# Kernel optimization log

Hardware: AMD Instinct MI355X
Metric: run time of the kernel (lower is better)

The kernel has to match this reference:

```python
import jax, jax.numpy as jnp
import numpy as np

B, S, D, H = 2, 2048, 1024, 16
HD = D // H  # head_dim = 64
NEG_INF = -jnp.inf


def _rope_tables(seq_len, head_dim, theta=10000.0):
    inv = 1.0 / (theta ** (np.arange(0, head_dim, 2, dtype=np.float32) / head_dim))
    t = np.arange(seq_len, dtype=np.float32)
    ang = np.outer(t, inv)  # [S, HD/2]
    return jnp.asarray(np.cos(ang)), jnp.asarray(np.sin(ang))


def _apply_rope(x, cos, sin):
    # x: [B, S, H, HD]; pairs (even, odd) rotated by complex freqs, matching
    # torch.view_as_complex(reshape(..., -1, 2)) * freqs_cis.
    x2 = x.reshape(*x.shape[:-1], HD // 2, 2)
    x0, x1 = x2[..., 0], x2[..., 1]
    c = cos[None, :, None, :]
    s = sin[None, :, None, :]
    o0 = x0 * c - x1 * s
    o1 = x0 * s + x1 * c
    return jnp.stack([o0, o1], axis=-1).reshape(x.shape)


def setup_inputs() -> dict:
    key = jax.random.key(0)
    ks = jax.random.split(key, 10)
    sc = 1.0 / np.sqrt(D)
    return {
        "x": jax.random.normal(ks[0], (B, S, D), dtype=jnp.float32),
        "effective_len": jax.random.randint(ks[1], (B,), 0, 1024, dtype=jnp.int32),
        "Wq": jax.random.normal(ks[2], (D, D), dtype=jnp.float32) * sc,
        "bq": jnp.zeros((D,), dtype=jnp.float32),
        "Wk": jax.random.normal(ks[3], (D, D), dtype=jnp.float32) * sc,
        "bk": jnp.zeros((D,), dtype=jnp.float32),
        "Wv": jax.random.normal(ks[4], (D, D), dtype=jnp.float32) * sc,
        "bv": jnp.zeros((D,), dtype=jnp.float32),
        "Wo": jax.random.normal(ks[5], (D, D), dtype=jnp.float32) * sc,
        "bo": jnp.zeros((D,), dtype=jnp.float32),
    }


def reference(x, effective_len, Wq, bq, Wk, bk, Wv, bv, Wo, bo):
    cos, sin = _rope_tables(S, HD)
    q = (x @ Wq.T + bq).reshape(B, S, H, HD)
    k = (x @ Wk.T + bk).reshape(B, S, H, HD)
    v = (x @ Wv.T + bv).reshape(B, S, H, HD)
    q = _apply_rope(q, cos, sin)
    k = _apply_rope(k, cos, sin)
    # [B, H, S, S]
    scores = jnp.einsum("bqhd,bkhd->bhqk", q, k) / np.sqrt(HD)
    row = jnp.arange(S)[:, None]
    col = jnp.arange(S)[None, :]
    causal = jnp.where(col > row, NEG_INF, 0.0)  # [S, S]
    scores = scores + causal[None, None, :, :]
    # faithful replication of original: masks the LAST effective_len key columns
    pad = jnp.where(col[None, 0, :] >= (S - effective_len)[:, None], NEG_INF, 0.0)  # [B, S]
    scores = scores + pad[:, None, None, :]
    probs = jax.nn.softmax(scores.astype(jnp.float32), axis=-1).astype(x.dtype)
    out = jnp.einsum("bhqk,bkhd->bqhd", probs, v).reshape(B, S, D)
    return out @ Wo.T + bo  # dropout in eval mode = identity
```

## Files before the change

### kernel.cpp

```cpp
#include <hip/hip_runtime.h>

#define SB   2048
#define DD   1024
#define NH   16
#define HDIM 64
#define NB   2

typedef float f4 __attribute__((ext_vector_type(4)));
typedef __bf16 bf16x8 __attribute__((ext_vector_type(8)));
typedef unsigned short u16;
typedef unsigned int u32;
typedef unsigned long long u64;
typedef u16 u16x8 __attribute__((ext_vector_type(8)));
typedef u16 u16x4 __attribute__((ext_vector_type(4)));

#define QSCALE 0.1803368801111f

__device__ __forceinline__ u16 f2bf(float f) {
  unsigned u = __float_as_uint(f);
  u += 0x7FFFu + ((u >> 16) & 1u);
  return (u16)(u >> 16);
}

typedef __attribute__((address_space(3))) unsigned int lds_uint;
typedef __attribute__((address_space(1))) const unsigned int glb_uint;
__device__ __forceinline__ void gl_lds16(const void* g, void* l) {
  __builtin_amdgcn_global_load_lds((glb_uint*)g, (lds_uint*)l, 16, 0, 0);
}

__device__ __forceinline__ void cvt8(const float* __restrict__ src,
                                     u16* __restrict__ dst, size_t i) {
  f4 a = *(const f4*)(src + 8 * i);
  f4 b = *(const f4*)(src + 8 * i + 4);
  u16x8 o;
  o[0] = f2bf(a[0]); o[1] = f2bf(a[1]); o[2] = f2bf(a[2]); o[3] = f2bf(a[3]);
  o[4] = f2bf(b[0]); o[5] = f2bf(b[1]); o[6] = f2bf(b[2]); o[7] = f2bf(b[3]);
  *(u16x8*)(dst + 8 * i) = o;
}

__global__ __launch_bounds__(256) void prep_kernel(
    const float* __restrict__ x, const float* __restrict__ Wq,
    const float* __restrict__ Wk, const float* __restrict__ Wv,
    const float* __restrict__ Wo,
    u16* __restrict__ xb, u16* __restrict__ Wb3, u16* __restrict__ WoB,
    float* __restrict__ cosT, float* __restrict__ sinT, int nwo) {
  int bid = blockIdx.x, t = threadIdx.x;
  if (bid < 2048) {
    cvt8(x, xb, (size_t)bid * 256 + t);
  } else if (bid < 2560) {
    cvt8(Wq, Wb3, (size_t)(bid - 2048) * 256 + t);
  } else if (bid < 3072) {
    cvt8(Wk, Wb3 + (1u << 20), (size_t)(bid - 2560) * 256 + t);
  } else if (bid < 3584) {
    cvt8(Wv, Wb3 + (2u << 20), (size_t)(bid - 3072) * 256 + t);
  } else if (bid < 3584 + nwo) {
    cvt8(Wo, WoB, (size_t)(bid - 3584) * 256 + t);
  } else {
    int idx = (bid - 3584 - nwo) * 256 + t;
    int tt = idx & 31, s = idx >> 5;
    float inv = powf(10000.0f, -2.0f * (float)tt / 64.0f);
    float ang = (float)s * inv;
    cosT[idx] = cosf(ang);
    sinT[idx] = sinf(ang);
  }
}

__global__ __launch_bounds__(256) void cvt_bf16_kernel(const float* __restrict__ src,
                                                       u16* __restrict__ dst) {
  cvt8(src, dst, (size_t)blockIdx.x * 256 + threadIdx.x);
}

__global__ __launch_bounds__(256, 4) void gemm_qkv_fused_kernel(
    const u16* __restrict__ A, const u16* __restrict__ W3,
    const float* __restrict__ bq, const float* __restrict__ bk,
    const float* __restrict__ bv,
    u16* __restrict__ Qw, u16* __restrict__ Kw, u16* __restrict__ Vt,
    const float* __restrict__ cosT, const float* __restrict__ sinT) {
  const int K = DD;
  __shared__ char smem[32768];
  u16* As = (u16*)smem;
  u16* Bs = (u16*)(smem + 16384);
  const int t = threadIdx.x;
  const int wave = t >> 6, lane = t & 63;
  const int m0 = blockIdx.x * 128, n0 = blockIdx.y * 128;
  const int mw = (wave >> 1) * 64, nw = (wave & 1) * 64;
  const int quad = lane >> 4, l15 = lane & 15;
  const int srow = lane >> 3, sgran = lane & 7;
  const u16* Ab = A + (size_t)m0 * K;
  const u16* Bb = W3 + (size_t)n0 * K;
  f4 acc[4][4];
#pragma unroll
  for (int i = 0; i < 4; i++)
#pragma unroll
    for (int j = 0; j < 4; j++) acc[i][j] = (f4)0.f;

  for (int kt = 0; kt < K; kt += 64) {
#pragma unroll
    for (int is = 0; is < 4; is++) {
      int r = wave * 32 + is * 8 + srow;
      int lg = sgran ^ (r & 7);
      gl_lds16(Ab + (size_t)r * K + kt + lg * 8, &As[(wave * 32 + is * 8) * 64]);
      gl_lds16(Bb + (size_t)r * K + kt + lg * 8, &Bs[(wave * 32 + is * 8) * 64]);
    }
    __syncthreads();
#pragma unroll
    for (int kh = 0; kh < 2; kh++) {
      bf16x8 af[4], bfr[4];
#pragma unroll
      for (int i = 0; i < 4; i++) {
        int R = mw + 16 * i + l15;
        af[i] = *(const bf16x8*)&As[R * 64 + ((kh * 4 + quad) ^ (R & 7)) * 8];
        int Rb = nw + 16 * i + l15;
        bfr[i] = *(const bf16x8*)&Bs[Rb * 64 + ((kh * 4 + quad) ^ (Rb & 7)) * 8];
      }
#pragma unroll
      for (int i = 0; i < 4; i++)
#pragma unroll
        for (int j = 0; j < 4; j++)
          acc[i][j] = __builtin_amdgcn_mfma_f32_16x16x32_bf16(af[i], bfr[j],
                                                              acc[i][j], 0, 0, 0);
    }
    __syncthreads();
  }

  const int which = n0 >> 10;
  const int hh = ((n0 & 1023) + nw) >> 6;
  const int cb = (n0 + nw) & 1023;

  if (which == 2) {
#pragma unroll
    for (int j = 0; j < 4; j++) {
      const int dh = 16 * j + l15;
      const float bval = bv[cb + 16 * j + l15];
#pragma unroll
      for (int a = 0; a < 2; a++) {
        int mg0 = m0 + mw + 32 * a;
        int b = mg0 >> 11, sr0 = mg0 & (SB - 1);
        u16x8 o;
#pragma unroll
        for (int r = 0; r < 4; r++) o[r] = f2bf(acc[2 * a][j][r] + bval);
#pragma unroll
        for (int r = 0; r < 4; r++) o[4 + r] = f2bf(acc[2 * a + 1][j][r] + bval);
        *(u16x8*)(Vt + ((size_t)(b * NH + hh) * HDIM + dh) * SB +
                  (sr0 | (quad << 3))) = o;
      }
    }
  } else {
    u16* dst = which ? Kw : Qw;
    const float* barr = which ? bk : bq;
    const float scale = which ? 1.0f : QSCALE;
    float bvj[4];
#pragma unroll
    for (int j = 0; j < 4; j++) bvj[j] = barr[cb + 16 * j + l15];
    float* sl = (float*)(smem + wave * 8192);
    const int kk = lane >> 1, hf = lane & 1;
#pragma unroll
    for (int half = 0; half < 2; half++) {
#pragma unroll
      for (int il = 0; il < 2; il++) {
#pragma unroll
        for (int j = 0; j < 4; j++) {
          const int q = 4 * j + (l15 >> 2);
          const int w = l15 & 3;
#pragma unroll
          for (int r = 0; r < 4; r++) {
            const int row = il * 16 + quad * 4 + r;
            sl[(row << 6) + (((q + row) & 15) << 2) + w] =
                (acc[half * 2 + il][j][r] + bvj[j]) * scale;
          }
        }
      }
      asm volatile("s_waitcnt lgkmcnt(0)" ::: "memory");
      const int m = m0 + mw + half * 32 + kk;
      const int b = m >> 11, sr = m & (SB - 1);
      const float* ct = cosT + sr * 32 + hf * 16;
      const float* st2 = sinT + sr * 32 + hf * 16;
      u16* op = dst + (((size_t)(b * NH + hh)) * SB + sr) * HDIM + hf * 32;
#pragma unroll
      for (int q8 = 0; q8 < 4; q8++) {
        f4 c4 = *(const f4*)(ct + q8 * 4);
        f4 s4 = *(const f4*)(st2 + q8 * 4);
        const int qc0 = hf * 8 + q8 * 2;
        f4 v0 = *(const f4*)(sl + (kk << 6) + (((qc0 + kk) & 15) << 2));
        f4 v1 = *(const f4*)(sl + (kk << 6) + (((qc0 + 1 + kk) & 15) << 2));
        u16x8 o;
        o[0] = f2bf(v0[0] * c4[0] - v0[1] * s4[0]);
        o[1] = f2bf(v0[0] * s4[0] + v0[1] * c4[0]);
        o[2] = f2bf(v0[2] * c4[1] - v0[3] * s4[1]);
        o[3] = f2bf(v0[2] * s4[1] + v0[3] * c4[1]);
        o[4] = f2bf(v1[0] * c4[2] - v1[1] * s4[2]);
        o[5] = f2bf(v1[0] * s4[2] + v1[1] * c4[2]);
        o[6] = f2bf(v1[2] * c4[3] - v1[3] * s4[3]);
        o[7] = f2bf(v1[2] * s4[3] + v1[3] * c4[3]);
        *(u16x8*)(op + q8 * 8) = o;
      }
      if (half == 0) asm volatile("s_waitcnt lgkmcnt(0)" ::: "memory");
    }
  }
}

__global__ __launch_bounds__(256) void gemm_out_kernel(
    const u16* __restrict__ A, const u16* __restrict__ W,
    const float* __restrict__ bias, float* __restrict__ outp) {
  const int K = DD;
  __shared__ u16 As[128 * 64];
  __shared__ u16 Bs[64 * 64];
  const int t = threadIdx.x;
  const int wave = t >> 6, lane = t & 63;
  const int m0 = blockIdx.x * 128, n0 = blockIdx.y * 64;
  const int mw = (wave >> 1) * 64, nw = (wave & 1) * 32;
  const int quad = lane >> 4, l15 = lane & 15;
  const int srow = lane >> 3, sgran = lane & 7;
  const u16* Ab = A + (size_t)m0 * K;
  const u16* Bb = W + (size_t)n0 * K;
  f4 acc[4][2];
#pragma unroll
  for (int i = 0; i < 4; i++)
#pragma unroll
    for (int j = 0; j < 2; j++) acc[i][j] = (f4)0.f;

  for (int kt = 0; kt < K; kt += 64) {
#pragma unroll
    for (int is = 0; is < 4; is++) {
      int r = wave * 32 + is * 8 + srow;
      int lg = sgran ^ (r & 7);
      gl_lds16(Ab + (size_t)r * K + kt + lg * 8, &As[(wave * 32 + is * 8) * 64]);
    }
#pragma unroll
    for (int is = 0; is < 2; is++) {
      int r = wave * 16 + is * 8 + srow;
      int lg = sgran ^ (r & 7);
      gl_lds16(Bb + (size_t)r * K + kt + lg * 8, &Bs[(wave * 16 + is * 8) * 64]);
    }
    __syncthreads();
#pragma unroll
    for (int kh = 0; kh < 2; kh++) {
      bf16x8 af[4], bfr[2];
#pragma unroll
      for (int i = 0; i < 4; i++) {
        int R = mw + 16 * i + l15;
        af[i] = *(const bf16x8*)&As[R * 64 + ((kh * 4 + quad) ^ (R & 7)) * 8];
      }
#pragma unroll
      for (int j = 0; j < 2; j++) {
        int R = nw + 16 * j + l15;
        bfr[j] = *(const bf16x8*)&Bs[R * 64 + ((kh * 4 + quad) ^ (R & 7)) * 8];
      }
#pragma unroll
      for (int i = 0; i < 4; i++)
#pragma unroll
        for (int j = 0; j < 2; j++)
          acc[i][j] = __builtin_amdgcn_mfma_f32_16x16x32_bf16(af[i], bfr[j],
                                                              acc[i][j], 0, 0, 0);
    }
    __syncthreads();
  }
#pragma unroll
  for (int i = 0; i < 4; i++)
#pragma unroll
    for (int j = 0; j < 2; j++) {
      int colg = n0 + nw + 16 * j + l15;
#pragma unroll
      for (int r = 0; r < 4; r++) {
        int mg = m0 + mw + 16 * i + quad * 4 + r;
        outp[(size_t)mg * DD + colg] = acc[i][j][r] + bias[colg];
      }
    }
}

__global__ __launch_bounds__(512) void attn_mfma_kernel(
    const u16* __restrict__ Qw, const u16* __restrict__ Kw,
    const u16* __restrict__ Vt, u16* __restrict__ Ow,
    const int* __restrict__ eff) {
  __shared__ u16 KL[2][8 * 64 * 8];
  __shared__ u16 VL[2][8 * 64 * 8];
  const int w = threadIdx.x >> 6, lane = threadIdx.x & 63;
  const int l15 = lane & 15, q4 = lane >> 4;
  const int lid = blockIdx.x;
  const int qp = lid >> 5;
  const int c  = lid & 31;
  const int h = c & 15, b = c >> 4;
  const int wg = w >> 2, wl = w & 3;
  const int QT = wg ? (SB / 128 - 1 - qp) : qp;
  const int limit = SB - eff[b];
  const size_t bh = ((size_t)b * NH + h) * (SB * HDIM);

  const int rowbase = QT * 128 + wl * 32;

  bf16x8 qf[2][2];
  {
    const u16* qp0 = Qw + bh + (size_t)(rowbase + l15) * HDIM + q4 * 8;
    qf[0][0] = *(const bf16x8*)qp0;
    qf[0][1] = *(const bf16x8*)(qp0 + 32);
    const u16* qp1 = qp0 + 16 * HDIM;
    qf[1][0] = *(const bf16x8*)qp1;
    qf[1][1] = *(const bf16x8*)(qp1 + 32);
  }

  f4 acc[2][4];
#pragma unroll
  for (int s = 0; s < 2; s++)
#pragma unroll
    for (int dt = 0; dt < 4; dt++) acc[s][dt] = (f4)0.f;
  float l_run[2] = {0.f, 0.f};

  const int kendB = min((SB / 128 - 1 - qp) * 128 + 127, limit - 1);
  const int ntiles = (kendB >> 6) + 1;
  const int wkend = min(rowbase + 31, limit - 1);

#define STAGE_TILE(TILE, BUF)                                                   \
  {                                                                             \
    const int colb_ = (TILE) * 64;                                              \
    _Pragma("unroll") for (int f = 0; f < 2; f++) {                             \
      int fr = w * 2 + f;                                                       \
      if (fr < 8) {                                                             \
        int mt = fr >> 1, j = fr & 1;                                           \
        gl_lds16(Kw + bh + (size_t)(colb_ + mt * 16 + l15) * HDIM + q4 * 8 + j * 32, \
                 &KL[BUF][fr * 512]);                                           \
      } else {                                                                  \
        int fv = fr - 8, dt = fv >> 1, j = fv & 1;                              \
        gl_lds16(Vt + bh + (size_t)(dt * 16 + l15) * SB + colb_ + q4 * 8 + j * 32, \
                 &VL[BUF][fv * 512]);                                           \
      }                                                                         \
    }                                                                           \
  }

  STAGE_TILE(0, 0)
  __syncthreads();

  for (int kt = 0; kt < ntiles; kt++) {
    const int cur = kt & 1;
    const int colb = kt * 64;
    if (kt + 1 < ntiles) STAGE_TILE(kt + 1, cur ^ 1)

    if (colb <= wkend) {
      f4 sa[2][4];
      __builtin_amdgcn_s_setprio(1);
#pragma unroll
      for (int mt = 0; mt < 4; mt++) {
        bf16x8 k0 = *(const bf16x8*)&KL[cur][(mt * 2 + 0) * 512 + lane * 8];
        bf16x8 k1 = *(const bf16x8*)&KL[cur][(mt * 2 + 1) * 512 + lane * 8];
        f4 s0 = (f4)0.f, s1 = (f4)0.f;
        s0 = __builtin_amdgcn_mfma_f32_16x16x32_bf16(k0, qf[0][0], s0, 0, 0, 0);
        s0 = __builtin_amdgcn_mfma_f32_16x16x32_bf16(k1, qf[0][1], s0, 0, 0, 0);
        s1 = __builtin_amdgcn_mfma_f32_16x16x32_bf16(k0, qf[1][0], s1, 0, 0, 0);
        s1 = __builtin_amdgcn_mfma_f32_16x16x32_bf16(k1, qf[1][1], s1, 0, 0, 0);
        sa[0][mt] = s0;
        sa[1][mt] = s1;
      }
      __builtin_amdgcn_s_setprio(0);

      u32 pk[2][4][2];
#pragma unroll
      for (int s = 0; s < 2; s++) {
        const int rb = rowbase + 16 * s;
        const int rg = rb + l15;
        const bool needmask = (colb + 63 > rb) || (colb + 63 >= limit);
        if (needmask) {
#pragma unroll
          for (int mt = 0; mt < 4; mt++)
#pragma unroll
            for (int r = 0; r < 4; r++) {
              int col = colb + mt * 16 + q4 * 4 + r;
              if (col > rg || col >= limit) sa[s][mt][r] = -3.0e38f;
            }
        }
        float lsum = 0.f;
#pragma unroll
        for (int mt = 0; mt < 4; mt++) {
          float p0 = exp2f(sa[s][mt][0]);
          float p1 = exp2f(sa[s][mt][1]);
          float p2 = exp2f(sa[s][mt][2]);
          float p3 = exp2f(sa[s][mt][3]);
          lsum += (p0 + p1) + (p2 + p3);
          pk[s][mt][0] = (__float_as_uint(p1) & 0xFFFF0000u) | (__float_as_uint(p0) >> 16);
          pk[s][mt][1] = (__float_as_uint(p3) & 0xFFFF0000u) | (__float_as_uint(p2) >> 16);
        }
        l_run[s] += lsum;
      }

      union { u32 wds[4]; bf16x8 v; } ub[2][2];
#pragma unroll
      for (int s = 0; s < 2; s++) {
        ub[s][0].wds[0] = pk[s][0][0]; ub[s][0].wds[1] = pk[s][0][1];
        ub[s][0].wds[2] = pk[s][1][0]; ub[s][0].wds[3] = pk[s][1][1];
        ub[s][1].wds[0] = pk[s][2][0]; ub[s][1].wds[1] = pk[s][2][1];
        ub[s][1].wds[2] = pk[s][3][0]; ub[s][1].wds[3] = pk[s][3][1];
      }
      __builtin_amdgcn_s_setprio(1);
#pragma unroll
      for (int dt = 0; dt < 4; dt++) {
        bf16x8 v0 = *(const bf16x8*)&VL[cur][(dt * 2 + 0) * 512 + lane * 8];
        bf16x8 v1 = *(const bf16x8*)&VL[cur][(dt * 2 + 1) * 512 + lane * 8];
#pragma unroll
        for (int s = 0; s < 2; s++) {
          acc[s][dt] = __builtin_amdgcn_mfma_f32_16x16x32_bf16(v0, ub[s][0].v, acc[s][dt], 0, 0, 0);
          acc[s][dt] = __builtin_amdgcn_mfma_f32_16x16x32_bf16(v1, ub[s][1].v, acc[s][dt], 0, 0, 0);
        }
      }
      __builtin_amdgcn_s_setprio(0);
    }
    __syncthreads();
  }

#pragma unroll
  for (int s = 0; s < 2; s++) {
    float lt = l_run[s];
    lt += __shfl_xor(lt, 16);
    lt += __shfl_xor(lt, 32);
    const float linv = 1.0f / lt;
    const int rg = rowbase + 16 * s + l15;
    const size_t obase = (((size_t)b * SB + rg) * NH + h) * HDIM + q4 * 4;
#pragma unroll
    for (int dt = 0; dt < 4; dt++) {
      u16x4 o;
      o[0] = f2bf(acc[s][dt][0] * linv);
      o[1] = f2bf(acc[s][dt][1] * linv);
      o[2] = f2bf(acc[s][dt][2] * linv);
      o[3] = f2bf(acc[s][dt][3] * linv);
      *(u16x4*)(Ow + obase + dt * 16) = o;
    }
  }
}

extern "C" void kernel_launch(void* const* d_in, const int* in_sizes, int n_in,
                              void* d_out, int out_size, void* d_ws, size_t ws_size,
                              hipStream_t stream) {
  (void)in_sizes; (void)n_in; (void)out_size;
  const float* x  = (const float*)d_in[0];
  const int*   eff = (const int*)d_in[1];
  const float* Wq = (const float*)d_in[2];
  const float* bq = (const float*)d_in[3];
  const float* Wk = (const float*)d_in[4];
  const float* bk = (const float*)d_in[5];
  const float* Wv = (const float*)d_in[6];
  const float* bv = (const float*)d_in[7];
  const float* Wo = (const float*)d_in[8];
  const float* bo = (const float*)d_in[9];
  float* out = (float*)d_out;

  char* ws = (char*)d_ws;
  u16* Qw = (u16*)(ws);
  u16* Kw = (u16*)(ws + (8u << 20));
  u16* Vt = (u16*)(ws + (16u << 20));
  u16* Ow = (u16*)(ws + (24u << 20));
  u16* xb = (u16*)(ws + (24u << 20));
  u16* Wb3 = (u16*)(ws + (32u << 20));
  float* cosT = (float*)(ws + (38u << 20));
  float* sinT = (float*)(ws + (38u << 20) + (256u << 10));

  size_t wob_off = (38u << 20) + (512u << 10);
  int nwo = (ws_size >= wob_off + (2u << 20)) ? 512 : 0;
  u16* WoB = nwo ? (u16*)(ws + wob_off) : Wb3;

  hipLaunchKernelGGL(prep_kernel, dim3(3840 + nwo), dim3(256), 0, stream,
                     x, Wq, Wk, Wv, Wo, xb, Wb3, WoB, cosT, sinT, nwo);

  hipLaunchKernelGGL(gemm_qkv_fused_kernel, dim3(32, 24), dim3(256), 0, stream,
                     xb, Wb3, bq, bk, bv, Qw, Kw, Vt, cosT, sinT);

  if (!nwo)
    hipLaunchKernelGGL(cvt_bf16_kernel, dim3(512), dim3(256), 0, stream, Wo, WoB);

  hipLaunchKernelGGL(attn_mfma_kernel, dim3(256), dim3(512), 0, stream,
                     Qw, Kw, Vt, Ow, eff);

  hipLaunchKernelGGL(gemm_out_kernel, dim3(32, 16), dim3(256), 0, stream, Ow, WoB, bo, out);
}
```

Baseline: 191.2 us.

## Double-buffer QKV GEMM LDS tiles with K-step 32 to overlap loads and MFMA

The fused QKV projection GEMM now uses two LDS buffers of 128x32 A/B tiles and prefetches the next K-slice while computing on the current one, instead of loading a 64-wide K tile and synchronizing before compute. The LDS swizzle changes to a 4-granule XOR pattern to match the narrower tiles. The goal is to hide global-to-LDS latency behind the MFMA work. In exchange there are twice as many loop iterations and barriers, and each iteration does less compute, which may not cover the load latency.

Result: slower. 198.9 us (+4.0%).

```diff
diff --git a/kernel.cpp b/kernel.cpp
--- a/kernel.cpp
+++ b/kernel.cpp
@@ -78,14 +78,12 @@
     const float* __restrict__ cosT, const float* __restrict__ sinT) {
   const int K = DD;
   __shared__ char smem[32768];
-  u16* As = (u16*)smem;
-  u16* Bs = (u16*)(smem + 16384);
   const int t = threadIdx.x;
   const int wave = t >> 6, lane = t & 63;
   const int m0 = blockIdx.x * 128, n0 = blockIdx.y * 128;
   const int mw = (wave >> 1) * 64, nw = (wave & 1) * 64;
   const int quad = lane >> 4, l15 = lane & 15;
-  const int srow = lane >> 3, sgran = lane & 7;
+  const int srow = lane >> 2, sgran = lane & 3;
   const u16* Ab = A + (size_t)m0 * K;
   const u16* Bb = W3 + (size_t)n0 * K;
   f4 acc[4][4];
@@ -94,32 +92,41 @@
 #pragma unroll
     for (int j = 0; j < 4; j++) acc[i][j] = (f4)0.f;
 
-  for (int kt = 0; kt < K; kt += 64) {
-#pragma unroll
-    for (int is = 0; is < 4; is++) {
-      int r = wave * 32 + is * 8 + srow;
-      int lg = sgran ^ (r & 7);
-      gl_lds16(Ab + (size_t)r * K + kt + lg * 8, &As[(wave * 32 + is * 8) * 64]);
-      gl_lds16(Bb + (size_t)r * K + kt + lg * 8, &Bs[(wave * 32 + is * 8) * 64]);
-    }
-    __syncthreads();
-#pragma unroll
-    for (int kh = 0; kh < 2; kh++) {
-      bf16x8 af[4], bfr[4];
-#pragma unroll
-      for (int i = 0; i < 4; i++) {
-        int R = mw + 16 * i + l15;
-        af[i] = *(const bf16x8*)&As[R * 64 + ((kh * 4 + quad) ^ (R & 7)) * 8];
-        int Rb = nw + 16 * i + l15;
-        bfr[i] = *(const bf16x8*)&Bs[Rb * 64 + ((kh * 4 + quad) ^ (Rb & 7)) * 8];
-      }
-#pragma unroll
-      for (int i = 0; i < 4; i++)
-#pragma unroll
-        for (int j = 0; j < 4; j++)
-          acc[i][j] = __builtin_amdgcn_mfma_f32_16x16x32_bf16(af[i], bfr[j],
-                                                              acc[i][j], 0, 0, 0);
-    }
+#define QKV_STAGE(KT, BUF)                                                \
+  {                                                                       \
+    u16* Asb_ = (u16*)(smem + (BUF) * 16384);                             \
+    u16* Bsb_ = (u16*)(smem + (BUF) * 16384 + 8192);                      \
+    _Pragma("unroll") for (int is = 0; is < 2; is++) {                    \
+      int r = wave * 32 + is * 16 + srow;                                 \
+      int lg = sgran ^ (r & 3);                                           \
+      gl_lds16(Ab + (size_t)r * K + (KT) * 32 + lg * 8,                   \
+               &Asb_[(wave * 32 + is * 16) * 32]);                        \
+      gl_lds16(Bb + (size_t)r * K + (KT) * 32 + lg * 8,                   \
+               &Bsb_[(wave * 32 + is * 16) * 32]);                        \
+    }                                                                     \
+  }
+
+  QKV_STAGE(0, 0)
+  __syncthreads();
+  for (int kt = 0; kt < 32; kt++) {
+    const int cur = kt & 1;
+    if (kt + 1 < 32) QKV_STAGE(kt + 1, cur ^ 1)
+    const u16* Asb = (const u16*)(smem + cur * 16384);
+    const u16* Bsb = (const u16*)(smem + cur * 16384 + 8192);
+    bf16x8 af[4], bfr[4];
+#pragma unroll
+    for (int i = 0; i < 4; i++) {
+      int R = mw + 16 * i + l15;
+      af[i] = *(const bf16x8*)&Asb[R * 32 + (quad ^ (R & 3)) * 8];
+      int Rb = nw + 16 * i + l15;
+      bfr[i] = *(const bf16x8*)&Bsb[Rb * 32 + (quad ^ (Rb & 3)) * 8];
+    }
+#pragma unroll
+    for (int i = 0; i < 4; i++)
+#pragma unroll
+      for (int j = 0; j < 4; j++)
+        acc[i][j] = __builtin_amdgcn_mfma_f32_16x16x32_bf16(af[i], bfr[j],
+                                                            acc[i][j], 0, 0, 0);
     __syncthreads();
   }
 
```

## Split attention query tiles across two blocks, one 16-row strip per wave

Applied to the files above, without the earlier changes.

The attention grid doubles from 256 to 512 blocks. Each block now covers half of a 128-row query pair, so each wave handles 16 query rows instead of 32. The goal is more blocks per GPU (256 CUs on MI355X) and lower per-wave register pressure, which should improve occupancy and load balance. In exchange, each K/V tile is staged into LDS twice as often across the grid, and there is less MFMA work per LDS read.

Result: no change. 189.8 us (-0.7%).

```diff
diff --git a/kernel.cpp b/kernel.cpp
--- a/kernel.cpp
+++ b/kernel.cpp
@@ -277,7 +277,8 @@
   const int w = threadIdx.x >> 6, lane = threadIdx.x & 63;
   const int l15 = lane & 15, q4 = lane >> 4;
   const int lid = blockIdx.x;
-  const int qp = lid >> 5;
+  const int qp = lid >> 6;
+  const int half = (lid >> 5) & 1;
   const int c  = lid & 31;
   const int h = c & 15, b = c >> 4;
   const int wg = w >> 2, wl = w & 3;
@@ -285,28 +286,23 @@
   const int limit = SB - eff[b];
   const size_t bh = ((size_t)b * NH + h) * (SB * HDIM);
 
-  const int rowbase = QT * 128 + wl * 32;
-
-  bf16x8 qf[2][2];
+  const int rowbase = QT * 128 + half * 64 + wl * 16;
+
+  bf16x8 qf[2];
   {
     const u16* qp0 = Qw + bh + (size_t)(rowbase + l15) * HDIM + q4 * 8;
-    qf[0][0] = *(const bf16x8*)qp0;
-    qf[0][1] = *(const bf16x8*)(qp0 + 32);
-    const u16* qp1 = qp0 + 16 * HDIM;
-    qf[1][0] = *(const bf16x8*)qp1;
-    qf[1][1] = *(const bf16x8*)(qp1 + 32);
-  }
-
-  f4 acc[2][4];
-#pragma unroll
-  for (int s = 0; s < 2; s++)
-#pragma unroll
-    for (int dt = 0; dt < 4; dt++) acc[s][dt] = (f4)0.f;
-  float l_run[2] = {0.f, 0.f};
+    qf[0] = *(const bf16x8*)qp0;
+    qf[1] = *(const bf16x8*)(qp0 + 32);
+  }
+
+  f4 acc[4];
+#pragma unroll
+  for (int dt = 0; dt < 4; dt++) acc[dt] = (f4)0.f;
+  float l_run = 0.f;
 
   const int kendB = min((SB / 128 - 1 - qp) * 128 + 127, limit - 1);
   const int ntiles = (kendB >> 6) + 1;
-  const int wkend = min(rowbase + 31, limit - 1);
+  const int wkend = min(rowbase + 15, limit - 1);
 
 #define STAGE_TILE(TILE, BUF)                                                   \
   {                                                                             \
@@ -334,90 +330,78 @@
     if (kt + 1 < ntiles) STAGE_TILE(kt + 1, cur ^ 1)
 
     if (colb <= wkend) {
-      f4 sa[2][4];
+      f4 sa[4];
       __builtin_amdgcn_s_setprio(1);
 #pragma unroll
       for (int mt = 0; mt < 4; mt++) {
         bf16x8 k0 = *(const bf16x8*)&KL[cur][(mt * 2 + 0) * 512 + lane * 8];
         bf16x8 k1 = *(const bf16x8*)&KL[cur][(mt * 2 + 1) * 512 + lane * 8];
-        f4 s0 = (f4)0.f, s1 = (f4)0.f;
-        s0 = __builtin_amdgcn_mfma_f32_16x16x32_bf16(k0, qf[0][0], s0, 0, 0, 0);
-        s0 = __builtin_amdgcn_mfma_f32_16x16x32_bf16(k1, qf[0][1], s0, 0, 0, 0);
-        s1 = __builtin_amdgcn_mfma_f32_16x16x32_bf16(k0, qf[1][0], s1, 0, 0, 0);
-        s1 = __builtin_amdgcn_mfma_f32_16x16x32_bf16(k1, qf[1][1], s1, 0, 0, 0);
-        sa[0][mt] = s0;
-        sa[1][mt] = s1;
+        f4 s0 = (f4)0.f;
+        s0 = __builtin_amdgcn_mfma_f32_16x16x32_bf16(k0, qf[0], s0, 0, 0, 0);
+        s0 = __builtin_amdgcn_mfma_f32_16x16x32_bf16(k1, qf[1], s0, 0, 0, 0);
+        sa[mt] = s0;
       }
       __builtin_amdgcn_s_setprio(0);
 
-      u32 pk[2][4][2];
-#pragma unroll
-      for (int s = 0; s < 2; s++) {
-        const int rb = rowbase + 16 * s;
-        const int rg = rb + l15;
-        const bool needmask = (colb + 63 > rb) || (colb + 63 >= limit);
+      u32 pk[4][2];
+      {
+        const int rg = rowbase + l15;
+        const bool needmask = (colb + 63 > rowbase) || (colb + 63 >= limit);
         if (needmask) {
 #pragma unroll
           for (int mt = 0; mt < 4; mt++)
 #pragma unroll
             for (int r = 0; r < 4; r++) {
               int col = colb + mt * 16 + q4 * 4 + r;
-              if (col > rg || col >= limit) sa[s][mt][r] = -3.0e38f;
+              if (col > rg || col >= limit) sa[mt][r] = -3.0e38f;
             }
         }
         float lsum = 0.f;
 #pragma unroll
         for (int mt = 0; mt < 4; mt++) {
-          float p0 = exp2f(sa[s][mt][0]);
-          float p1 = exp2f(sa[s][mt][1]);
-          float p2 = exp2f(sa[s][mt][2]);
-          float p3 = exp2f(sa[s][mt][3]);
+          float p0 = exp2f(sa[mt][0]);
+          float p1 = exp2f(sa[mt][1]);
+          float p2 = exp2f(sa[mt][2]);
+          float p3 = exp2f(sa[mt][3]);
           lsum += (p0 + p1) + (p2 + p3);
-          pk[s][mt][0] = (__float_as_uint(p1) & 0xFFFF0000u) | (__float_as_uint(p0) >> 16);
-          pk[s][mt][1] = (__float_as_uint(p3) & 0xFFFF0000u) | (__float_as_uint(p2) >> 16);
+          pk[mt][0] = (__float_as_uint(p1) & 0xFFFF0000u) | (__float_as_uint(p0) >> 16);
+          pk[mt][1] = (__float_as_uint(p3) & 0xFFFF0000u) | (__float_as_uint(p2) >> 16);
         }
-        l_run[s] += lsum;
-      }
-
-      union { u32 wds[4]; bf16x8 v; } ub[2][2];
-#pragma unroll
-      for (int s = 0; s < 2; s++) {
-        ub[s][0].wds[0] = pk[s][0][0]; ub[s][0].wds[1] = pk[s][0][1];
-        ub[s][0].wds[2] = pk[s][1][0]; ub[s][0].wds[3] = pk[s][1][1];
-        ub[s][1].wds[0] = pk[s][2][0]; ub[s][1].wds[1] = pk[s][2][1];
-        ub[s][1].wds[2] = pk[s][3][0]; ub[s][1].wds[3] = pk[s][3][1];
-      }
+        l_run += lsum;
+      }
+
+      union { u32 wds[4]; bf16x8 v; } ub0, ub1;
+      ub0.wds[0] = pk[0][0]; ub0.wds[1] = pk[0][1];
+      ub0.wds[2] = pk[1][0]; ub0.wds[3] = pk[1][1];
+      ub1.wds[0] = pk[2][0]; ub1.wds[1] = pk[2][1];
+      ub1.wds[2] = pk[3][0]; ub1.wds[3] = pk[3][1];
       __builtin_amdgcn_s_setprio(1);
 #pragma unroll
       for (int dt = 0; dt < 4; dt++) {
         bf16x8 v0 = *(const bf16x8*)&VL[cur][(dt * 2 + 0) * 512 + lane * 8];
         bf16x8 v1 = *(const bf16x8*)&VL[cur][(dt * 2 + 1) * 512 + lane * 8];
-#pragma unroll
-        for (int s = 0; s < 2; s++) {
-          acc[s][dt] = __builtin_amdgcn_mfma_f32_16x16x32_bf16(v0, ub[s][0].v, acc[s][dt], 0, 0, 0);
-          acc[s][dt] = __builtin_amdgcn_mfma_f32_16x16x32_bf16(v1, ub[s][1].v, acc[s][dt], 0, 0, 0);
-        }
+        acc[dt] = __builtin_amdgcn_mfma_f32_16x16x32_bf16(v0, ub0.v, acc[dt], 0, 0, 0);
+        acc[dt] = __builtin_amdgcn_mfma_f32_16x16x32_bf16(v1, ub1.v, acc[dt], 0, 0, 0);
       }
       __builtin_amdgcn_s_setprio(0);
     }
     __syncthreads();
   }
 
-#pragma unroll
-  for (int s = 0; s < 2; s++) {
-    float lt = l_run[s];
+  {
+    float lt = l_run;
     lt += __shfl_xor(lt, 16);
     lt += __shfl_xor(lt, 32);
     const float linv = 1.0f / lt;
-    const int rg = rowbase + 16 * s + l15;
+    const int rg = rowbase + l15;
     const size_t obase = (((size_t)b * SB + rg) * NH + h) * HDIM + q4 * 4;
 #pragma unroll
     for (int dt = 0; dt < 4; dt++) {
       u16x4 o;
-      o[0] = f2bf(acc[s][dt][0] * linv);
-      o[1] = f2bf(acc[s][dt][1] * linv);
-      o[2] = f2bf(acc[s][dt][2] * linv);
-      o[3] = f2bf(acc[s][dt][3] * linv);
+      o[0] = f2bf(acc[dt][0] * linv);
+      o[1] = f2bf(acc[dt][1] * linv);
+      o[2] = f2bf(acc[dt][2] * linv);
+      o[3] = f2bf(acc[dt][3] * linv);
       *(u16x4*)(Ow + obase + dt * 16) = o;
     }
   }
@@ -462,7 +446,7 @@
   if (!nwo)
     hipLaunchKernelGGL(cvt_bf16_kernel, dim3(512), dim3(256), 0, stream, Wo, WoB);
 
-  hipLaunchKernelGGL(attn_mfma_kernel, dim3(256), dim3(512), 0, stream,
+  hipLaunchKernelGGL(attn_mfma_kernel, dim3(512), dim3(512), 0, stream,
                      Qw, Kw, Vt, Ow, eff);
 
   hipLaunchKernelGGL(gemm_out_kernel, dim3(32, 16), dim3(256), 0, stream, Ow, WoB, bo, out);
```
